# Optimization experiments

Hardware: AMD Instinct MI355X
Metric: run time of the kernel (lower is better)

## Reference

```python
import jax, jax.numpy as jnp
import numpy as np

E = 256        # emb_size / d_model
DI = 512       # d_inner = expand * d_model
N = 16         # d_state
R = 16         # dt_rank = ceil(E/16)
KC = 4         # d_conv


def layer_norm(x, g, b, eps=1e-5):
    m = jnp.mean(x, axis=-1, keepdims=True)
    v = jnp.mean((x - m) ** 2, axis=-1, keepdims=True)
    return (x - m) * jax.lax.rsqrt(v + eps) * g + b


def causal_dw_conv(x, w, b):
    # x: (B,T,DI), w: (DI,KC), b: (DI). torch Conv1d(groups=DI, padding=KC-1)[..., :T]
    T = x.shape[1]
    xp = jnp.pad(x, ((0, 0), (KC - 1, 0), (0, 0)))
    y = sum(xp[:, k:k + T, :] * w[None, None, :, k] for k in range(KC))
    return y + b


def selective_scan(u, dt, A, Bm, Cm, D):
    # u,dt: (B,T,DI); A: (DI,N); Bm,Cm: (B,T,N); D: (DI,)
    dA = jnp.exp(dt[..., None] * A)                       # (B,T,DI,N)
    dBu = dt[..., None] * Bm[:, :, None, :] * u[..., None]

    def step(h, inp):
        dA_t, dBu_t, C_t = inp
        h = dA_t * h + dBu_t                              # (B,DI,N)
        y = jnp.einsum('bdn,bn->bd', h, C_t)
        return h, y

    h0 = jnp.zeros((u.shape[0], DI, N), u.dtype)
    _, ys = jax.lax.scan(step, h0, (jnp.swapaxes(dA, 0, 1), jnp.swapaxes(dBu, 0, 1), jnp.swapaxes(Cm, 0, 1)))
    return jnp.swapaxes(ys, 0, 1) + u * D


def mamba(x, W_in, conv_w, conv_b, W_xproj, W_dt, b_dt, A_log, Dp, W_out):
    xz = x @ W_in.T                                       # (B,T,2*DI)
    xm, z = xz[..., :DI], xz[..., DI:]
    xm = jax.nn.silu(causal_dw_conv(xm, conv_w, conv_b))
    xdbl = xm @ W_xproj.T                                 # (B,T,R+2N)
    dt = jax.nn.softplus(xdbl[..., :R] @ W_dt.T + b_dt)   # (B,T,DI)
    Bm, Cm = xdbl[..., R:R + N], xdbl[..., R + N:]
    A = -jnp.exp(A_log)
    y = selective_scan(xm, dt, A, Bm, Cm, Dp)
    return (y * jax.nn.silu(z)) @ W_out.T


def forward(f_wavlm, f_sinc, ln_w_g, ln_w_b, ln_s_g, ln_s_b, W_wp, b_wp, W_sp, b_sp,
            W_fuse, b_fuse, W_se1, W_se2, ln_f_g, ln_f_b,
            n1_g, n1_b, n2_g, n2_b,
            W_in, conv_w, conv_b, W_xproj, W_dt, b_dt, A_log, Dp, W_out,
            W_ff1, b_ff1, W_ff2, b_ff2):
    # DualStreamFusion
    fw = layer_norm(f_wavlm, ln_w_g, ln_w_b) @ W_wp.T + b_wp   # (B,T1,E)
    fs = layer_norm(f_sinc, ln_s_g, ln_s_b) @ W_sp.T + b_sp    # (B,T2,E)
    B, T1, _ = fw.shape
    # F.interpolate(mode='linear', align_corners=False) == half-pixel linear resize
    fs = jax.image.resize(fs, (B, T1, E), method='linear')
    fc = jnp.concatenate([fw, fs], axis=-1) @ W_fuse.T + b_fuse
    # SE layer
    se = jax.nn.sigmoid(jax.nn.relu(jnp.mean(fc, axis=1) @ W_se1.T) @ W_se2.T)
    fc = fc * se[:, None, :]
    x = layer_norm(fc, ln_f_g, ln_f_b)                          # dropout is eval identity
    # PN_BiMambas_Encoder
    res = x
    xn = layer_norm(x, n1_g, n1_b)
    mp = (W_in, conv_w, conv_b, W_xproj, W_dt, b_dt, A_log, Dp, W_out)
    mf = mamba(xn, *mp)
    mb = jnp.flip(mamba(jnp.flip(xn, axis=1), *mp), axis=1)
    m = layer_norm(mf + mb, n2_g, n2_b)
    ff = jax.nn.gelu(m @ W_ff1.T + b_ff1, approximate=False) @ W_ff2.T + b_ff2
    return ff + res


def setup_inputs() -> dict:
    key = jax.random.key(0)
    ks = jax.random.split(key, 24)
    g = lambda k, s: (jax.random.normal(k, s, jnp.float32) * 0.02)
    d = {
        'f_wavlm': jax.random.normal(ks[0], (4, 1024, 1024), jnp.float32),
        'f_sinc': jax.random.normal(ks[1], (4, 512, 64), jnp.float32),
        'ln_w_g': jnp.ones((1024,)), 'ln_w_b': jnp.zeros((1024,)),
        'ln_s_g': jnp.ones((64,)), 'ln_s_b': jnp.zeros((64,)),
        'W_wp': g(ks[2], (E, 1024)), 'b_wp': jnp.zeros((E,)),
        'W_sp': g(ks[3], (E, 64)), 'b_sp': jnp.zeros((E,)),
        'W_fuse': g(ks[4], (E, 2 * E)), 'b_fuse': jnp.zeros((E,)),
        'W_se1': g(ks[5], (E // 16, E)), 'W_se2': g(ks[6], (E, E // 16)),
        'ln_f_g': jnp.ones((E,)), 'ln_f_b': jnp.zeros((E,)),
        'n1_g': jnp.ones((E,)), 'n1_b': jnp.zeros((E,)),
        'n2_g': jnp.ones((E,)), 'n2_b': jnp.zeros((E,)),
        'W_in': g(ks[7], (2 * DI, E)),
        'conv_w': g(ks[8], (DI, KC)), 'conv_b': jnp.zeros((DI,)),
        'W_xproj': g(ks[9], (R + 2 * N, DI)),
        'W_dt': g(ks[10], (DI, R)), 'b_dt': jnp.full((DI,), -4.6, jnp.float32),
        'A_log': jnp.broadcast_to(jnp.log(jnp.arange(1, N + 1, dtype=jnp.float32)), (DI, N)).copy(),
        'Dp': jnp.ones((DI,)),
        'W_out': g(ks[11], (E, DI)),
        'W_ff1': g(ks[12], (4 * E, E)), 'b_ff1': jnp.zeros((4 * E,)),
        'W_ff2': g(ks[13], (E, 4 * E)), 'b_ff2': jnp.zeros((E,)),
    }
    return d


def reference(f_wavlm, f_sinc, ln_w_g, ln_w_b, ln_s_g, ln_s_b, W_wp, b_wp, W_sp, b_sp,
              W_fuse, b_fuse, W_se1, W_se2, ln_f_g, ln_f_b,
              n1_g, n1_b, n2_g, n2_b,
              W_in, conv_w, conv_b, W_xproj, W_dt, b_dt, A_log, Dp, W_out,
              W_ff1, b_ff1, W_ff2, b_ff2):
    return forward(f_wavlm, f_sinc, ln_w_g, ln_w_b, ln_s_g, ln_s_b, W_wp, b_wp, W_sp, b_sp,
                   W_fuse, b_fuse, W_se1, W_se2, ln_f_g, ln_f_b,
                   n1_g, n1_b, n2_g, n2_b,
                   W_in, conv_w, conv_b, W_xproj, W_dt, b_dt, A_log, Dp, W_out,
                   W_ff1, b_ff1, W_ff2, b_ff2)
```

## Files before the change

### kernel.cpp

```cpp
#include <hip/hip_runtime.h>
#include <math.h>

#define DEV_INLINE __device__ __forceinline__

typedef __attribute__((ext_vector_type(8))) short bf16x8;
typedef __attribute__((ext_vector_type(4))) float f32x4;

struct US4 { unsigned short x, y, z, w; };

DEV_INLINE unsigned short f2bf(float f) {
  union { float f; unsigned u; } v; v.f = f;
  unsigned r = v.u + 0x7fff + ((v.u >> 16) & 1);
  return (unsigned short)(r >> 16);
}
DEV_INLINE float bf2f(unsigned short h) {
  union { unsigned u; float f; } v; v.u = ((unsigned)h) << 16;
  return v.f;
}
DEV_INLINE float softplusf(float x) {
  return x > 20.f ? x : __logf(1.f + __expf(x));
}

static constexpr size_t OFF_XZ   = 0;
static constexpr size_t SUB_LNW  = 0;
static constexpr size_t SUB_LNS  = 2097152;
static constexpr size_t SUB_CAT  = 2162688;
static constexpr size_t SUB_FSB  = 3211264;
static constexpr size_t OFF_UB   = 4194304;
static constexpr size_t OFF_XD   = 6291456;
static constexpr size_t OFF_SP   = 6684672;
static constexpr size_t OFF_SH   = 8781824;
static constexpr size_t OFF_FC   = 10878976;
static constexpr size_t OFF_RES  = 11927552;
static constexpr size_t OFF_XNB  = 12976128;
static constexpr size_t OFF_MB   = 13500416;
static constexpr size_t OFF_FF1B = 14024704;
static constexpr size_t OFF_WB   = 16121856;
static constexpr size_t OFF_SE1  = 16797696;
static constexpr size_t OFF_SE2  = 16814080;

static constexpr size_t WB_WP    = 0;
static constexpr size_t WB_SP    = 262144;
static constexpr size_t WB_FUSE  = 278528;
static constexpr size_t WB_IN    = 409600;
static constexpr size_t WB_XPROJ = 671744;
static constexpr size_t WB_OUT   = 696320;
static constexpr size_t WB_FF1   = 827392;
static constexpr size_t WB_FF2   = 1089536;

__global__ void k_w2bf(const float* __restrict__ w0, const float* __restrict__ w1,
                       const float* __restrict__ w2, const float* __restrict__ w3,
                       const float* __restrict__ w4, const float* __restrict__ w5,
                       const float* __restrict__ w6, const float* __restrict__ w7,
                       unsigned short* __restrict__ dst) {
  int i = blockIdx.x * 256 + threadIdx.x;
  const float* s; size_t dbase; int rel;
  if      (i <  65536) { s = w0; rel = i;          dbase = WB_WP; }
  else if (i <  69632) { s = w1; rel = i -  65536; dbase = WB_SP; }
  else if (i < 102400) { s = w2; rel = i -  69632; dbase = WB_FUSE; }
  else if (i < 167936) { s = w3; rel = i - 102400; dbase = WB_IN; }
  else if (i < 174080) { s = w4; rel = i - 167936; dbase = WB_XPROJ; }
  else if (i < 206848) { s = w5; rel = i - 174080; dbase = WB_OUT; }
  else if (i < 272384) { s = w6; rel = i - 206848; dbase = WB_FF1; }
  else                 { s = w7; rel = i - 272384; dbase = WB_FF2; }
  float4 v = reinterpret_cast<const float4*>(s)[rel];
  US4 o = { f2bf(v.x), f2bf(v.y), f2bf(v.z), f2bf(v.w) };
  reinterpret_cast<US4*>(dst + dbase)[rel] = o;
}

DEV_INLINE float blockSum256(float v) {
  __shared__ float sh[4];
  int lane = threadIdx.x & 63;
  int w    = threadIdx.x >> 6;
#pragma unroll
  for (int o = 32; o; o >>= 1) v += __shfl_down(v, o, 64);
  __syncthreads();
  if (lane == 0) sh[w] = v;
  __syncthreads();
  return sh[0] + sh[1] + sh[2] + sh[3];
}

__global__ void k_layernorm(const float* __restrict__ in, unsigned short* __restrict__ out,
                            const float* __restrict__ g, const float* __restrict__ b,
                            int L) {
  __shared__ float row[1024];
  size_t rid = blockIdx.x;
  const float* x = in + rid * (size_t)L;
  float s = 0.f;
  for (int i = threadIdx.x; i < L; i += 256) { float v = x[i]; row[i] = v; s += v; }
  float mean = blockSum256(s) / (float)L;
  float vs = 0.f;
  for (int i = threadIdx.x; i < L; i += 256) { float d = row[i] - mean; vs += d * d; }
  float var = blockSum256(vs) / (float)L;
  float rstd = rsqrtf(var + 1e-5f);
  for (int i = threadIdx.x; i < L; i += 256)
    out[rid * (size_t)L + i] = f2bf((row[i] - mean) * rstd * g[i] + b[i]);
}

__global__ void k_layernorm2(const float* __restrict__ mo, unsigned short* __restrict__ out,
                             const float* __restrict__ g, const float* __restrict__ b) {
  size_t rid = blockIdx.x;
  int e = threadIdx.x;
  float v = mo[rid * 256 + e] + mo[(rid + 4096) * 256 + e];
  float m1 = blockSum256(v) * (1.f / 256.f);
  float d = v - m1;
  float var = blockSum256(d * d) * (1.f / 256.f);
  out[rid * 256 + e] = f2bf(d * rsqrtf(var + 1e-5f) * g[e] + b[e]);
}

template <int ACT, bool RESADD, bool OUTBF>
__global__ __launch_bounds__(128) void k_mgemm(
    const short* __restrict__ A, int lda,
    const short* __restrict__ W, int ldw,
    const float* __restrict__ bias,
    float* __restrict__ Cf, unsigned short* __restrict__ Cb, int ldc,
    const float* __restrict__ res,
    int M, int N, int K) {
  int l = threadIdx.x & 63, w = threadIdx.x >> 6;
  int bm = blockIdx.y << 6, bn = blockIdx.x << 6;
  int r = l & 15, ko = (l >> 4) << 3;
  const short* Ap = A + (size_t)(bm + (w << 5) + r) * lda + ko;
  const short* Wp = W + (size_t)(bn + r) * ldw + ko;
  f32x4 acc[2][4] = {{{0.f,0.f,0.f,0.f},{0.f,0.f,0.f,0.f},{0.f,0.f,0.f,0.f},{0.f,0.f,0.f,0.f}},
                     {{0.f,0.f,0.f,0.f},{0.f,0.f,0.f,0.f},{0.f,0.f,0.f,0.f},{0.f,0.f,0.f,0.f}}};
#pragma unroll 2
  for (int k0 = 0; k0 < K; k0 += 32) {
    bf16x8 a0 = *reinterpret_cast<const bf16x8*>(Ap + k0);
    bf16x8 a1 = *reinterpret_cast<const bf16x8*>(Ap + (size_t)16 * lda + k0);
#pragma unroll
    for (int t = 0; t < 4; t++) {
      if (bn + t * 16 < N) {
        bf16x8 bv = *reinterpret_cast<const bf16x8*>(Wp + (size_t)(t * 16) * ldw + k0);
        acc[0][t] = __builtin_amdgcn_mfma_f32_16x16x32_bf16(a0, bv, acc[0][t], 0, 0, 0);
        acc[1][t] = __builtin_amdgcn_mfma_f32_16x16x32_bf16(a1, bv, acc[1][t], 0, 0, 0);
      }
    }
  }
#pragma unroll
  for (int mf = 0; mf < 2; mf++) {
#pragma unroll
    for (int t = 0; t < 4; t++) {
      if (bn + t * 16 < N) {
        int n = bn + t * 16 + r;
        float bb = bias ? bias[n] : 0.f;
#pragma unroll
        for (int q = 0; q < 4; q++) {
          int m = bm + (w << 5) + (mf << 4) + ((l >> 4) << 2) + q;
          float v = acc[mf][t][q] + bb;
          if (ACT == 1) v = 0.5f * v * (1.f + erff(v * 0.70710678118f));
          size_t oi = (size_t)m * ldc + n;
          if (OUTBF) {
            Cb[oi] = f2bf(v);
          } else {
            if (RESADD) v += res[oi];
            Cf[oi] = v;
          }
        }
      }
    }
  }
}

__global__ void k_resize(const unsigned short* __restrict__ fs,
                         unsigned short* __restrict__ cat) {
  int idx = blockIdx.x * 256 + threadIdx.x;
  int e = idx & 255, t = (idx >> 8) & 1023, b = idx >> 18;
  int j = t >> 1;
  int j0, j1; float w0, w1;
  if ((t & 1) == 0) { j0 = j > 0 ? j - 1 : 0; j1 = j; w0 = 0.25f; w1 = 0.75f; }
  else              { j0 = j; j1 = j < 511 ? j + 1 : 511; w0 = 0.75f; w1 = 0.25f; }
  float v = w0 * bf2f(fs[((size_t)(b << 9) + j0) * 256 + e]) +
            w1 * bf2f(fs[((size_t)(b << 9) + j1) * 256 + e]);
  cat[((size_t)(b << 10) + t) * 512 + 256 + e] = f2bf(v);
}

__global__ void k_se_part(const float* __restrict__ fc, float* __restrict__ part) {
  int b = blockIdx.y, chunk = blockIdx.x, e = threadIdx.x;
  float s = 0.f;
  for (int j = 0; j < 64; j++) {
    int t = chunk * 64 + j;
    s += fc[((size_t)(b << 10) + t) * 256 + e];
  }
  part[(size_t)(b * 16 + chunk) * 256 + e] = s;
}

__global__ void k_se_fin(const float* __restrict__ part, const float* __restrict__ W1,
                         const float* __restrict__ W2, float* __restrict__ se) {
  int b = blockIdx.x, tid = threadIdx.x;
  __shared__ float mean[256];
  __shared__ float hid[16];
  float s = 0.f;
  for (int c = 0; c < 16; c++) s += part[(size_t)(b * 16 + c) * 256 + tid];
  mean[tid] = s * (1.f / 1024.f);
  __syncthreads();
  int o = tid >> 4, l = tid & 15;
  float p = 0.f;
  for (int e = l; e < 256; e += 16) p += mean[e] * W1[o * 256 + e];
  p += __shfl_xor(p, 1, 64); p += __shfl_xor(p, 2, 64);
  p += __shfl_xor(p, 4, 64); p += __shfl_xor(p, 8, 64);
  if (l == 0) hid[o] = fmaxf(p, 0.f);
  __syncthreads();
  float s2 = 0.f;
  for (int o2 = 0; o2 < 16; o2++) s2 += hid[o2] * W2[tid * 16 + o2];
  se[b * 256 + tid] = 1.f / (1.f + expf(-s2));
}

__global__ void k_se_ln(const float* __restrict__ fc, const float* __restrict__ se,
                        const float* __restrict__ gf, const float* __restrict__ bf,
                        const float* __restrict__ g1, const float* __restrict__ b1,
                        float* __restrict__ xout, unsigned short* __restrict__ xnb) {
  size_t rid = blockIdx.x;
  int b = (int)(rid >> 10);
  int e = threadIdx.x;
  float v = fc[rid * 256 + e] * se[b * 256 + e];
  float m1 = blockSum256(v) * (1.f / 256.f);
  float d = v - m1;
  float var = blockSum256(d * d) * (1.f / 256.f);
  float x = d * rsqrtf(var + 1e-5f) * gf[e] + bf[e];
  xout[rid * 256 + e] = x;
  float m2 = blockSum256(x) * (1.f / 256.f);
  float d2 = x - m2;
  float v2 = blockSum256(d2 * d2) * (1.f / 256.f);
  xnb[rid * 256 + e] = f2bf(d2 * rsqrtf(v2 + 1e-5f) * g1[e] + b1[e]);
}

__global__ void k_conv(const float* __restrict__ xz, const float* __restrict__ cw,
                       const float* __restrict__ cb, unsigned short* __restrict__ ub) {
  int idx = blockIdx.x * 256 + threadIdx.x;
  int d4 = idx & 127, t = (idx >> 7) & 1023, b = idx >> 17;
  int base = d4 << 2;
  f32x4 rr[7];
#pragma unroll
  for (int o = 0; o < 7; o++) {
    int tt = t + o - 3;
    if (tt >= 0 && tt < 1024)
      rr[o] = *reinterpret_cast<const f32x4*>(xz + ((size_t)(b << 10) + tt) * 1024 + base);
    else
      rr[o] = (f32x4){0.f, 0.f, 0.f, 0.f};
  }
  f32x4 wv[4];
#pragma unroll
  for (int dd = 0; dd < 4; dd++)
    wv[dd] = *reinterpret_cast<const f32x4*>(cw + (size_t)(base + dd) * 4);
  f32x4 cbv = *reinterpret_cast<const f32x4*>(cb + base);
  f32x4 acc0 = cbv, acc1 = cbv;
#pragma unroll
  for (int k = 0; k < 4; k++) {
#pragma unroll
    for (int dd = 0; dd < 4; dd++) {
      acc0[dd] += rr[k][dd] * wv[dd][k];
      acc1[dd] += rr[6 - k][dd] * wv[dd][k];
    }
  }
  US4 o0, o1;
  {
    float v0 = acc0[0] / (1.f + expf(-acc0[0]));
    float v1 = acc0[1] / (1.f + expf(-acc0[1]));
    float v2 = acc0[2] / (1.f + expf(-acc0[2]));
    float v3 = acc0[3] / (1.f + expf(-acc0[3]));
    o0 = { f2bf(v0), f2bf(v1), f2bf(v2), f2bf(v3) };
    v0 = acc1[0] / (1.f + expf(-acc1[0]));
    v1 = acc1[1] / (1.f + expf(-acc1[1]));
    v2 = acc1[2] / (1.f + expf(-acc1[2]));
    v3 = acc1[3] / (1.f + expf(-acc1[3]));
    o1 = { f2bf(v0), f2bf(v1), f2bf(v2), f2bf(v3) };
  }
  size_t r0 = ((size_t)(b << 10) + t) * 512 + base;
  size_t r1 = ((size_t)((4 + b) << 10) + t) * 512 + base;
  *reinterpret_cast<US4*>(ub + r0) = o0;
  *reinterpret_cast<US4*>(ub + r1) = o1;
}


__global__ __launch_bounds__(256) void k_scan_a(
    const unsigned short* __restrict__ ub, const float* __restrict__ xdbl,
    const float* __restrict__ A_log, const float* __restrict__ Wdt,
    const float* __restrict__ bdt,
    float* __restrict__ SP, float* __restrict__ SH) {
  int chunk = blockIdx.x, b = blockIdx.y;
  int dir = blockIdx.z >> 1, dhalf = blockIdx.z & 1;
  int d = (dhalf << 8) + threadIdx.x;
  __shared__ float Ds[32][16];
  __shared__ float Bs[32][16];
  for (int i = threadIdx.x; i < 512; i += 256) {
    int j = i >> 4, n = i & 15;
    int s = (chunk << 5) + j;
    int t = dir ? (1023 - s) : s;
    size_t row = ((size_t)((dir * 4 + b) * 1024 + t)) * 48;
    Ds[j][n] = xdbl[row + n];
    Bs[j][n] = xdbl[row + 16 + n];
  }
  float a[16], h[16], P[16], wdt[16];
#pragma unroll
  for (int n = 0; n < 16; n++) {
    a[n] = -__expf(A_log[d * 16 + n]);
    wdt[n] = Wdt[d * 16 + n];
    h[n] = 0.f; P[n] = 1.f;
  }
  float dbias = bdt[d];
  __syncthreads();
  size_t base = (size_t)(dir * 4 + b) * 1024;
  int s0 = chunk << 5;
#define ADDR(j) ((base + (dir ? (1023 - (s0 + (j))) : (s0 + (j)))) * 512 + d)
  float u_n = bf2f(ub[ADDR(0)]);
#pragma unroll 4
  for (int j = 0; j < 32; j++) {
    float uv = u_n;
    if (j < 31) u_n = bf2f(ub[ADDR(j + 1)]);
    float sdt = dbias;
#pragma unroll
    for (int rj = 0; rj < 16; rj++) sdt += Ds[j][rj] * wdt[rj];
    float dtv = softplusf(sdt);
    float c1 = dtv * uv;
    const float4* Bp = reinterpret_cast<const float4*>(&Bs[j][0]);
    float4 b0 = Bp[0], b1 = Bp[1], b2 = Bp[2], b3 = Bp[3];
    float Bv[16] = {b0.x, b0.y, b0.z, b0.w, b1.x, b1.y, b1.z, b1.w,
                    b2.x, b2.y, b2.z, b2.w, b3.x, b3.y, b3.z, b3.w};
#pragma unroll
    for (int n = 0; n < 16; n++) {
      float dA = __expf(dtv * a[n]);
      h[n] = dA * h[n] + c1 * Bv[n];
      P[n] *= dA;
    }
  }
  size_t o = ((size_t)((dir * 4 + b) * 32 + chunk) * 512 + d) * 16;
#pragma unroll
  for (int n = 0; n < 16; n++) { SP[o + n] = P[n]; SH[o + n] = h[n]; }
#undef ADDR
}

__global__ __launch_bounds__(256) void k_scan_mid(float* __restrict__ SP,
                                                  const float* __restrict__ SH) {
  int dir = blockIdx.z, b = blockIdx.y;
  int d = (blockIdx.x << 4) + (threadIdx.x >> 4);
  int n = threadIdx.x & 15;
  const size_t cs = 512 * 16;
  size_t base = ((size_t)(dir * 4 + b) * 32) * cs + (size_t)d * 16 + n;
  float H = 0.f;
  float Pv = SP[base], hE = SH[base];
  for (int c = 0; c < 32; c++) {
    float Pc = Pv, hc = hE;
    if (c < 31) { Pv = SP[base + (c + 1) * cs]; hE = SH[base + (c + 1) * cs]; }
    SP[base + (size_t)c * cs] = H;
    H = Pc * H + hc;
  }
}

__global__ __launch_bounds__(256) void k_scan_b(
    unsigned short* __restrict__ ub, const float* __restrict__ xdbl,
    const float* __restrict__ A_log, const float* __restrict__ Wdt,
    const float* __restrict__ bdt, const float* __restrict__ Dp,
    const float* __restrict__ xz, const float* __restrict__ SP) {
  int chunk = blockIdx.x, b = blockIdx.y;
  int dir = blockIdx.z >> 1, dhalf = blockIdx.z & 1;
  int d = (dhalf << 8) + threadIdx.x;
  __shared__ float Ds[32][16];
  __shared__ float Bs[32][16];
  __shared__ float Cs[32][16];
  for (int i = threadIdx.x; i < 512; i += 256) {
    int j = i >> 4, n = i & 15;
    int s = (chunk << 5) + j;
    int t = dir ? (1023 - s) : s;
    size_t row = ((size_t)((dir * 4 + b) * 1024 + t)) * 48;
    Ds[j][n] = xdbl[row + n];
    Bs[j][n] = xdbl[row + 16 + n];
    Cs[j][n] = xdbl[row + 32 + n];
  }
  float a[16], h[16], wdt[16];
  size_t so = ((size_t)((dir * 4 + b) * 32 + chunk) * 512 + d) * 16;
#pragma unroll
  for (int n = 0; n < 16; n++) {
    a[n] = -__expf(A_log[d * 16 + n]);
    wdt[n] = Wdt[d * 16 + n];
    h[n] = SP[so + n];
  }
  float dbias = bdt[d];
  float Dval = Dp[d];
  __syncthreads();
  size_t base = (size_t)(dir * 4 + b) * 1024;
  size_t zbase = (size_t)b << 10;
  int s0 = chunk << 5;
#define ADDR(j) ((base + (dir ? (1023 - (s0 + (j))) : (s0 + (j)))) * 512 + d)
#define ZADDR(j) ((((zbase + (dir ? (1023 - (s0 + (j))) : (s0 + (j)))) << 10)) + 512 + d)
  float u_n = bf2f(ub[ADDR(0)]);
  float z_n = xz[ZADDR(0)];
#pragma unroll 4
  for (int j = 0; j < 32; j++) {
    float uv = u_n, zv = z_n;
    if (j < 31) { u_n = bf2f(ub[ADDR(j + 1)]); z_n = xz[ZADDR(j + 1)]; }
    float sdt = dbias;
#pragma unroll
    for (int rj = 0; rj < 16; rj++) sdt += Ds[j][rj] * wdt[rj];
    float dtv = softplusf(sdt);
    float c1 = dtv * uv;
    const float4* Bp = reinterpret_cast<const float4*>(&Bs[j][0]);
    const float4* Cp = reinterpret_cast<const float4*>(&Cs[j][0]);
    float4 b0 = Bp[0], b1 = Bp[1], b2 = Bp[2], b3 = Bp[3];
    float4 c0 = Cp[0], c4 = Cp[1], c8 = Cp[2], cc = Cp[3];
    float Bv[16] = {b0.x, b0.y, b0.z, b0.w, b1.x, b1.y, b1.z, b1.w,
                    b2.x, b2.y, b2.z, b2.w, b3.x, b3.y, b3.z, b3.w};
    float Cv[16] = {c0.x, c0.y, c0.z, c0.w, c4.x, c4.y, c4.z, c4.w,
                    c8.x, c8.y, c8.z, c8.w, cc.x, cc.y, cc.z, cc.w};
    float y0 = 0.f, y1 = 0.f, y2 = 0.f, y3 = 0.f;
#pragma unroll
    for (int n = 0; n < 16; n++) {
      float dA = __expf(dtv * a[n]);
      h[n] = dA * h[n] + c1 * Bv[n];
      float p = h[n] * Cv[n];
      if ((n & 3) == 0) y0 += p; else if ((n & 3) == 1) y1 += p;
      else if ((n & 3) == 2) y2 += p; else y3 += p;
    }
    float y = (y0 + y1) + (y2 + y3) + uv * Dval;
    float sig = 1.f / (1.f + expf(-zv));
    ub[ADDR(j)] = f2bf(y * zv * sig);
  }
#undef ADDR
#undef ZADDR
}

static inline void mgemm(hipStream_t st, int act, bool resadd, bool outbf,
                         const void* A, int lda, const void* W, int ldw,
                         const float* bias, void* Cf, void* Cb, int ldc,
                         const float* res, int M, int N, int K) {
  dim3 g((N + 63) / 64, M / 64), bl(128);
  const short* a = (const short*)A;
  const short* w = (const short*)W;
  float* cf = (float*)Cf;
  unsigned short* cb = (unsigned short*)Cb;
  if (outbf) {
    if (act == 1) hipLaunchKernelGGL((k_mgemm<1, false, true>), g, bl, 0, st, a, lda, w, ldw, bias, cf, cb, ldc, res, M, N, K);
    else          hipLaunchKernelGGL((k_mgemm<0, false, true>), g, bl, 0, st, a, lda, w, ldw, bias, cf, cb, ldc, res, M, N, K);
  } else {
    if (resadd)   hipLaunchKernelGGL((k_mgemm<0, true, false>), g, bl, 0, st, a, lda, w, ldw, bias, cf, cb, ldc, res, M, N, K);
    else          hipLaunchKernelGGL((k_mgemm<0, false, false>), g, bl, 0, st, a, lda, w, ldw, bias, cf, cb, ldc, res, M, N, K);
  }
}

extern "C" void kernel_launch(void* const* d_in, const int* in_sizes, int n_in,
                              void* d_out, int out_size, void* d_ws, size_t ws_size,
                              hipStream_t stream) {
  const float* f_wavlm = (const float*)d_in[0];
  const float* f_sinc  = (const float*)d_in[1];
  const float* ln_w_g  = (const float*)d_in[2];
  const float* ln_w_b  = (const float*)d_in[3];
  const float* ln_s_g  = (const float*)d_in[4];
  const float* ln_s_b  = (const float*)d_in[5];
  const float* W_wp    = (const float*)d_in[6];
  const float* b_wp    = (const float*)d_in[7];
  const float* W_sp    = (const float*)d_in[8];
  const float* b_sp    = (const float*)d_in[9];
  const float* W_fuse  = (const float*)d_in[10];
  const float* b_fuse  = (const float*)d_in[11];
  const float* W_se1   = (const float*)d_in[12];
  const float* W_se2   = (const float*)d_in[13];
  const float* ln_f_g  = (const float*)d_in[14];
  const float* ln_f_b  = (const float*)d_in[15];
  const float* n1_g    = (const float*)d_in[16];
  const float* n1_b    = (const float*)d_in[17];
  const float* n2_g    = (const float*)d_in[18];
  const float* n2_b    = (const float*)d_in[19];
  const float* W_in    = (const float*)d_in[20];
  const float* conv_w  = (const float*)d_in[21];
  const float* conv_b  = (const float*)d_in[22];
  const float* W_xproj = (const float*)d_in[23];
  const float* W_dt    = (const float*)d_in[24];
  const float* b_dt    = (const float*)d_in[25];
  const float* A_log   = (const float*)d_in[26];
  const float* Dp      = (const float*)d_in[27];
  const float* W_out   = (const float*)d_in[28];
  const float* W_ff1   = (const float*)d_in[29];
  const float* b_ff1   = (const float*)d_in[30];
  const float* W_ff2   = (const float*)d_in[31];
  const float* b_ff2   = (const float*)d_in[32];

  float* ws = (float*)d_ws;
  float* pXZ  = ws + OFF_XZ;
  unsigned short* pLNW = (unsigned short*)(ws + SUB_LNW);
  unsigned short* pLNS = (unsigned short*)(ws + SUB_LNS);
  unsigned short* pCAT = (unsigned short*)(ws + SUB_CAT);
  unsigned short* pFSB = (unsigned short*)(ws + SUB_FSB);
  unsigned short* pUB  = (unsigned short*)(ws + OFF_UB);
  float* pXD  = ws + OFF_XD;
  float* pSP  = ws + OFF_SP;
  float* pMO  = ws + OFF_SP;
  float* pSH  = ws + OFF_SH;
  float* pFC  = ws + OFF_FC;
  float* pRES = ws + OFF_RES;
  unsigned short* pXNB  = (unsigned short*)(ws + OFF_XNB);
  unsigned short* pMB   = (unsigned short*)(ws + OFF_MB);
  unsigned short* pFF1B = (unsigned short*)(ws + OFF_FF1B);
  unsigned short* pWB   = (unsigned short*)(ws + OFF_WB);
  float* pSE1 = ws + OFF_SE1;
  float* pSE2 = ws + OFF_SE2;

  hipLaunchKernelGGL(k_w2bf, dim3(1320), dim3(256), 0, stream,
                     W_wp, W_sp, W_fuse, W_in, W_xproj, W_out, W_ff1, W_ff2, pWB);

  hipLaunchKernelGGL(k_layernorm, dim3(4096), dim3(256), 0, stream,
                     f_wavlm, pLNW, ln_w_g, ln_w_b, 1024);
  mgemm(stream, 0, false, true, pLNW, 1024, pWB + WB_WP, 1024, b_wp,
        nullptr, pCAT, 512, nullptr, 4096, 256, 1024);

  hipLaunchKernelGGL(k_layernorm, dim3(2048), dim3(256), 0, stream,
                     f_sinc, pLNS, ln_s_g, ln_s_b, 64);
  mgemm(stream, 0, false, true, pLNS, 64, pWB + WB_SP, 64, b_sp,
        nullptr, pFSB, 256, nullptr, 2048, 256, 64);

  hipLaunchKernelGGL(k_resize, dim3(4096), dim3(256), 0, stream, pFSB, pCAT);
  mgemm(stream, 0, false, false, pCAT, 512, pWB + WB_FUSE, 512, b_fuse,
        pFC, nullptr, 256, nullptr, 4096, 256, 512);

  hipLaunchKernelGGL(k_se_part, dim3(16, 4), dim3(256), 0, stream, pFC, pSE1);
  hipLaunchKernelGGL(k_se_fin, dim3(4), dim3(256), 0, stream, pSE1, W_se1, W_se2, pSE2);

  hipLaunchKernelGGL(k_se_ln, dim3(4096), dim3(256), 0, stream,
                     pFC, pSE2, ln_f_g, ln_f_b, n1_g, n1_b, pRES, pXNB);

  mgemm(stream, 0, false, false, pXNB, 256, pWB + WB_IN, 256, nullptr,
        pXZ, nullptr, 1024, nullptr, 4096, 1024, 256);

  hipLaunchKernelGGL(k_conv, dim3(2048), dim3(256), 0, stream,
                     pXZ, conv_w, conv_b, pUB);

  mgemm(stream, 0, false, false, pUB, 512, pWB + WB_XPROJ, 512, nullptr,
        pXD, nullptr, 48, nullptr, 8192, 48, 512);

  hipLaunchKernelGGL(k_scan_a, dim3(32, 4, 4), dim3(256), 0, stream,
                     pUB, pXD, A_log, W_dt, b_dt, pSP, pSH);
  hipLaunchKernelGGL(k_scan_mid, dim3(32, 4, 2), dim3(256), 0, stream, pSP, pSH);
  hipLaunchKernelGGL(k_scan_b, dim3(32, 4, 4), dim3(256), 0, stream,
                     pUB, pXD, A_log, W_dt, b_dt, Dp, pXZ, pSP);

  mgemm(stream, 0, false, false, pUB, 512, pWB + WB_OUT, 512, nullptr,
        pMO, nullptr, 256, nullptr, 8192, 256, 512);
  hipLaunchKernelGGL(k_layernorm2, dim3(4096), dim3(256), 0, stream, pMO, pMB, n2_g, n2_b);

  mgemm(stream, 1, false, true, pMB, 256, pWB + WB_FF1, 256, b_ff1,
        nullptr, pFF1B, 1024, nullptr, 4096, 1024, 256);
  mgemm(stream, 0, true, false, pFF1B, 1024, pWB + WB_FF2, 1024, b_ff2,
        d_out, nullptr, 256, pRES, 4096, 256, 1024);
}
```

Measured before the change: 402.0 us.

## Split GEMM K across waves with LDS reduction; fuse z-silu into in-proj epilogue

The MFMA GEMM now uses 256-thread blocks. It splits the K dimension across 4 waves (or 2 waves for small K) and reduces the partial accumulators through shared memory, which adds waves per output tile and improves latency hiding. The in-projection GEMM gains a split output mode: the xm half goes to fp32 and silu(z) goes to a bf16 buffer, so the scan's final kernel reads half the bytes and skips the sigmoid. The costs are extra LDS traffic and a __syncthreads per tile. The K=64 GEMM with KS=2 and the N=48 case depend on the guard logic.

```diff
diff --git a/kernel.cpp b/kernel.cpp
--- a/kernel.cpp
+++ b/kernel.cpp
@@ -26,6 +26,8 @@
 static constexpr size_t SUB_LNS  = 2097152;
 static constexpr size_t SUB_CAT  = 2162688;
 static constexpr size_t SUB_FSB  = 3211264;
+static constexpr size_t SUB_XM   = 0;
+static constexpr size_t SUB_ZB   = 2097152;
 static constexpr size_t OFF_UB   = 4194304;
 static constexpr size_t OFF_XD   = 6291456;
 static constexpr size_t OFF_SP   = 6684672;
@@ -108,23 +110,28 @@
   out[rid * 256 + e] = f2bf(d * rsqrtf(var + 1e-5f) * g[e] + b[e]);
 }
 
-template <int ACT, bool RESADD, bool OUTBF>
-__global__ __launch_bounds__(128) void k_mgemm(
+template <int ACT, bool RESADD, int OUTMODE, int KS>
+__global__ __launch_bounds__(256) void k_mgemm(
     const short* __restrict__ A, int lda,
     const short* __restrict__ W, int ldw,
     const float* __restrict__ bias,
     float* __restrict__ Cf, unsigned short* __restrict__ Cb, int ldc,
     const float* __restrict__ res,
     int M, int N, int K) {
+  __shared__ float red[(KS == 2 ? 2 : 3)][32][65];
   int l = threadIdx.x & 63, w = threadIdx.x >> 6;
-  int bm = blockIdx.y << 6, bn = blockIdx.x << 6;
-  int r = l & 15, ko = (l >> 4) << 3;
-  const short* Ap = A + (size_t)(bm + (w << 5) + r) * lda + ko;
-  const short* Wp = W + (size_t)(bn + r) * ldw + ko;
+  int wm = (KS == 2) ? (w & 1) : 0;
+  int wk = (KS == 2) ? (w >> 1) : w;
+  int bm = (KS == 2) ? ((blockIdx.y << 6) + (wm << 5)) : (blockIdx.y << 5);
+  int bn = blockIdx.x << 6;
+  int r = l & 15, rrow = (l >> 4) << 2, ko = (l >> 4) << 3;
+  int KH = K / KS;
+  const short* Ap = A + (size_t)(bm + r) * lda + wk * KH + ko;
+  const short* Wp = W + (size_t)(bn + r) * ldw + wk * KH + ko;
   f32x4 acc[2][4] = {{{0.f,0.f,0.f,0.f},{0.f,0.f,0.f,0.f},{0.f,0.f,0.f,0.f},{0.f,0.f,0.f,0.f}},
                      {{0.f,0.f,0.f,0.f},{0.f,0.f,0.f,0.f},{0.f,0.f,0.f,0.f},{0.f,0.f,0.f,0.f}}};
 #pragma unroll 2
-  for (int k0 = 0; k0 < K; k0 += 32) {
+  for (int k0 = 0; k0 < KH; k0 += 32) {
     bf16x8 a0 = *reinterpret_cast<const bf16x8*>(Ap + k0);
     bf16x8 a1 = *reinterpret_cast<const bf16x8*>(Ap + (size_t)16 * lda + k0);
 #pragma unroll
@@ -136,24 +143,44 @@
       }
     }
   }
-#pragma unroll
-  for (int mf = 0; mf < 2; mf++) {
-#pragma unroll
-    for (int t = 0; t < 4; t++) {
-      if (bn + t * 16 < N) {
-        int n = bn + t * 16 + r;
-        float bb = bias ? bias[n] : 0.f;
-#pragma unroll
-        for (int q = 0; q < 4; q++) {
-          int m = bm + (w << 5) + (mf << 4) + ((l >> 4) << 2) + q;
-          float v = acc[mf][t][q] + bb;
-          if (ACT == 1) v = 0.5f * v * (1.f + erff(v * 0.70710678118f));
-          size_t oi = (size_t)m * ldc + n;
-          if (OUTBF) {
-            Cb[oi] = f2bf(v);
-          } else {
-            if (RESADD) v += res[oi];
-            Cf[oi] = v;
+  if (wk > 0) {
+    int slot = (KS == 2) ? wm : (wk - 1);
+#pragma unroll
+    for (int mf = 0; mf < 2; mf++)
+#pragma unroll
+      for (int t = 0; t < 4; t++)
+#pragma unroll
+        for (int q = 0; q < 4; q++)
+          red[slot][(mf << 4) + rrow + q][t * 16 + r] = acc[mf][t][q];
+  }
+  __syncthreads();
+  if (wk == 0) {
+#pragma unroll
+    for (int mf = 0; mf < 2; mf++) {
+#pragma unroll
+      for (int t = 0; t < 4; t++) {
+        if (bn + t * 16 < N) {
+          int n = bn + t * 16 + r;
+          float bb = bias ? bias[n] : 0.f;
+#pragma unroll
+          for (int q = 0; q < 4; q++) {
+            int rw = (mf << 4) + rrow + q, cl = t * 16 + r;
+            float v = acc[mf][t][q];
+            if (KS == 2) v += red[wm][rw][cl];
+            else         v += red[0][rw][cl] + red[1][rw][cl] + red[2][rw][cl];
+            v += bb;
+            if (ACT == 1) v = 0.5f * v * (1.f + erff(v * 0.70710678118f));
+            int m = bm + rw;
+            if (OUTMODE == 0) {
+              size_t oi = (size_t)m * ldc + n;
+              if (RESADD) v += res[oi];
+              Cf[oi] = v;
+            } else if (OUTMODE == 1) {
+              Cb[(size_t)m * ldc + n] = f2bf(v);
+            } else {
+              if (n < 512) Cf[(size_t)m * 512 + n] = v;
+              else Cb[(size_t)m * 512 + (n - 512)] = f2bf(v / (1.f + __expf(-v)));
+            }
           }
         }
       }
@@ -224,7 +251,7 @@
   xnb[rid * 256 + e] = f2bf(d2 * rsqrtf(v2 + 1e-5f) * g1[e] + b1[e]);
 }
 
-__global__ void k_conv(const float* __restrict__ xz, const float* __restrict__ cw,
+__global__ void k_conv(const float* __restrict__ xm, const float* __restrict__ cw,
                        const float* __restrict__ cb, unsigned short* __restrict__ ub) {
   int idx = blockIdx.x * 256 + threadIdx.x;
   int d4 = idx & 127, t = (idx >> 7) & 1023, b = idx >> 17;
@@ -234,7 +261,7 @@
   for (int o = 0; o < 7; o++) {
     int tt = t + o - 3;
     if (tt >= 0 && tt < 1024)
-      rr[o] = *reinterpret_cast<const f32x4*>(xz + ((size_t)(b << 10) + tt) * 1024 + base);
+      rr[o] = *reinterpret_cast<const f32x4*>(xm + ((size_t)(b << 10) + tt) * 512 + base);
     else
       rr[o] = (f32x4){0.f, 0.f, 0.f, 0.f};
   }
@@ -270,7 +297,6 @@
   *reinterpret_cast<US4*>(ub + r0) = o0;
   *reinterpret_cast<US4*>(ub + r1) = o1;
 }
-
 
 __global__ __launch_bounds__(256) void k_scan_a(
     const unsigned short* __restrict__ ub, const float* __restrict__ xdbl,
@@ -350,7 +376,7 @@
     unsigned short* __restrict__ ub, const float* __restrict__ xdbl,
     const float* __restrict__ A_log, const float* __restrict__ Wdt,
     const float* __restrict__ bdt, const float* __restrict__ Dp,
-    const float* __restrict__ xz, const float* __restrict__ SP) {
+    const unsigned short* __restrict__ zb, const float* __restrict__ SP) {
   int chunk = blockIdx.x, b = blockIdx.y;
   int dir = blockIdx.z >> 1, dhalf = blockIdx.z & 1;
   int d = (dhalf << 8) + threadIdx.x;
@@ -381,13 +407,13 @@
   size_t zbase = (size_t)b << 10;
   int s0 = chunk << 5;
 #define ADDR(j) ((base + (dir ? (1023 - (s0 + (j))) : (s0 + (j)))) * 512 + d)
-#define ZADDR(j) ((((zbase + (dir ? (1023 - (s0 + (j))) : (s0 + (j)))) << 10)) + 512 + d)
+#define ZADDR(j) (((zbase + (dir ? (1023 - (s0 + (j))) : (s0 + (j)))) * 512) + d)
   float u_n = bf2f(ub[ADDR(0)]);
-  float z_n = xz[ZADDR(0)];
+  float z_n = bf2f(zb[ZADDR(0)]);
 #pragma unroll 4
   for (int j = 0; j < 32; j++) {
-    float uv = u_n, zv = z_n;
-    if (j < 31) { u_n = bf2f(ub[ADDR(j + 1)]); z_n = xz[ZADDR(j + 1)]; }
+    float uv = u_n, szv = z_n;
+    if (j < 31) { u_n = bf2f(ub[ADDR(j + 1)]); z_n = bf2f(zb[ZADDR(j + 1)]); }
     float sdt = dbias;
 #pragma unroll
     for (int rj = 0; rj < 16; rj++) sdt += Ds[j][rj] * wdt[rj];
@@ -411,28 +437,31 @@
       else if ((n & 3) == 2) y2 += p; else y3 += p;
     }
     float y = (y0 + y1) + (y2 + y3) + uv * Dval;
-    float sig = 1.f / (1.f + expf(-zv));
-    ub[ADDR(j)] = f2bf(y * zv * sig);
+    ub[ADDR(j)] = f2bf(y * szv);
   }
 #undef ADDR
 #undef ZADDR
 }
 
-static inline void mgemm(hipStream_t st, int act, bool resadd, bool outbf,
+static inline void mgemm(hipStream_t st, int act, bool resadd, int outmode,
                          const void* A, int lda, const void* W, int ldw,
                          const float* bias, void* Cf, void* Cb, int ldc,
                          const float* res, int M, int N, int K) {
-  dim3 g((N + 63) / 64, M / 64), bl(128);
+  bool ks4 = (K >= 256);
+  dim3 g((N + 63) / 64, ks4 ? (M / 32) : (M / 64)), bl(256);
   const short* a = (const short*)A;
   const short* w = (const short*)W;
   float* cf = (float*)Cf;
   unsigned short* cb = (unsigned short*)Cb;
-  if (outbf) {
-    if (act == 1) hipLaunchKernelGGL((k_mgemm<1, false, true>), g, bl, 0, st, a, lda, w, ldw, bias, cf, cb, ldc, res, M, N, K);
-    else          hipLaunchKernelGGL((k_mgemm<0, false, true>), g, bl, 0, st, a, lda, w, ldw, bias, cf, cb, ldc, res, M, N, K);
+  if (outmode == 2) {
+    hipLaunchKernelGGL((k_mgemm<0, false, 2, 4>), g, bl, 0, st, a, lda, w, ldw, bias, cf, cb, ldc, res, M, N, K);
+  } else if (outmode == 1) {
+    if (act == 1)      hipLaunchKernelGGL((k_mgemm<1, false, 1, 4>), g, bl, 0, st, a, lda, w, ldw, bias, cf, cb, ldc, res, M, N, K);
+    else if (ks4)      hipLaunchKernelGGL((k_mgemm<0, false, 1, 4>), g, bl, 0, st, a, lda, w, ldw, bias, cf, cb, ldc, res, M, N, K);
+    else               hipLaunchKernelGGL((k_mgemm<0, false, 1, 2>), g, bl, 0, st, a, lda, w, ldw, bias, cf, cb, ldc, res, M, N, K);
   } else {
-    if (resadd)   hipLaunchKernelGGL((k_mgemm<0, true, false>), g, bl, 0, st, a, lda, w, ldw, bias, cf, cb, ldc, res, M, N, K);
-    else          hipLaunchKernelGGL((k_mgemm<0, false, false>), g, bl, 0, st, a, lda, w, ldw, bias, cf, cb, ldc, res, M, N, K);
+    if (resadd)        hipLaunchKernelGGL((k_mgemm<0, true, 0, 4>), g, bl, 0, st, a, lda, w, ldw, bias, cf, cb, ldc, res, M, N, K);
+    else               hipLaunchKernelGGL((k_mgemm<0, false, 0, 4>), g, bl, 0, st, a, lda, w, ldw, bias, cf, cb, ldc, res, M, N, K);
   }
 }
 
@@ -474,11 +503,12 @@
   const float* b_ff2   = (const float*)d_in[32];
 
   float* ws = (float*)d_ws;
-  float* pXZ  = ws + OFF_XZ;
   unsigned short* pLNW = (unsigned short*)(ws + SUB_LNW);
   unsigned short* pLNS = (unsigned short*)(ws + SUB_LNS);
   unsigned short* pCAT = (unsigned short*)(ws + SUB_CAT);
   unsigned short* pFSB = (unsigned short*)(ws + SUB_FSB);
+  float* pXM = ws + SUB_XM;
+  unsigned short* pZB = (unsigned short*)(ws + SUB_ZB);
   unsigned short* pUB  = (unsigned short*)(ws + OFF_UB);
   float* pXD  = ws + OFF_XD;
   float* pSP  = ws + OFF_SP;
@@ -498,16 +528,16 @@
 
   hipLaunchKernelGGL(k_layernorm, dim3(4096), dim3(256), 0, stream,
                      f_wavlm, pLNW, ln_w_g, ln_w_b, 1024);
-  mgemm(stream, 0, false, true, pLNW, 1024, pWB + WB_WP, 1024, b_wp,
+  mgemm(stream, 0, false, 1, pLNW, 1024, pWB + WB_WP, 1024, b_wp,
         nullptr, pCAT, 512, nullptr, 4096, 256, 1024);
 
   hipLaunchKernelGGL(k_layernorm, dim3(2048), dim3(256), 0, stream,
                      f_sinc, pLNS, ln_s_g, ln_s_b, 64);
-  mgemm(stream, 0, false, true, pLNS, 64, pWB + WB_SP, 64, b_sp,
+  mgemm(stream, 0, false, 1, pLNS, 64, pWB + WB_SP, 64, b_sp,
         nullptr, pFSB, 256, nullptr, 2048, 256, 64);
 
   hipLaunchKernelGGL(k_resize, dim3(4096), dim3(256), 0, stream, pFSB, pCAT);
-  mgemm(stream, 0, false, false, pCAT, 512, pWB + WB_FUSE, 512, b_fuse,
+  mgemm(stream, 0, false, 0, pCAT, 512, pWB + WB_FUSE, 512, b_fuse,
         pFC, nullptr, 256, nullptr, 4096, 256, 512);
 
   hipLaunchKernelGGL(k_se_part, dim3(16, 4), dim3(256), 0, stream, pFC, pSE1);
@@ -516,27 +546,27 @@
   hipLaunchKernelGGL(k_se_ln, dim3(4096), dim3(256), 0, stream,
                      pFC, pSE2, ln_f_g, ln_f_b, n1_g, n1_b, pRES, pXNB);
 
-  mgemm(stream, 0, false, false, pXNB, 256, pWB + WB_IN, 256, nullptr,
-        pXZ, nullptr, 1024, nullptr, 4096, 1024, 256);
+  mgemm(stream, 0, false, 2, pXNB, 256, pWB + WB_IN, 256, nullptr,
+        pXM, pZB, 512, nullptr, 4096, 1024, 256);
 
   hipLaunchKernelGGL(k_conv, dim3(2048), dim3(256), 0, stream,
-                     pXZ, conv_w, conv_b, pUB);
-
-  mgemm(stream, 0, false, false, pUB, 512, pWB + WB_XPROJ, 512, nullptr,
+                     pXM, conv_w, conv_b, pUB);
+
+  mgemm(stream, 0, false, 0, pUB, 512, pWB + WB_XPROJ, 512, nullptr,
         pXD, nullptr, 48, nullptr, 8192, 48, 512);
 
   hipLaunchKernelGGL(k_scan_a, dim3(32, 4, 4), dim3(256), 0, stream,
                      pUB, pXD, A_log, W_dt, b_dt, pSP, pSH);
   hipLaunchKernelGGL(k_scan_mid, dim3(32, 4, 2), dim3(256), 0, stream, pSP, pSH);
   hipLaunchKernelGGL(k_scan_b, dim3(32, 4, 4), dim3(256), 0, stream,
-                     pUB, pXD, A_log, W_dt, b_dt, Dp, pXZ, pSP);
-
-  mgemm(stream, 0, false, false, pUB, 512, pWB + WB_OUT, 512, nullptr,
+                     pUB, pXD, A_log, W_dt, b_dt, Dp, pZB, pSP);
+
+  mgemm(stream, 0, false, 0, pUB, 512, pWB + WB_OUT, 512, nullptr,
         pMO, nullptr, 256, nullptr, 8192, 256, 512);
   hipLaunchKernelGGL(k_layernorm2, dim3(4096), dim3(256), 0, stream, pMO, pMB, n2_g, n2_b);
 
-  mgemm(stream, 1, false, true, pMB, 256, pWB + WB_FF1, 256, b_ff1,
+  mgemm(stream, 1, false, 1, pMB, 256, pWB + WB_FF1, 256, b_ff1,
         nullptr, pFF1B, 1024, nullptr, 4096, 1024, 256);
-  mgemm(stream, 0, true, false, pFF1B, 1024, pWB + WB_FF2, 1024, b_ff2,
+  mgemm(stream, 0, true, 0, pFF1B, 1024, pWB + WB_FF2, 1024, b_ff2,
         d_out, nullptr, 256, pRES, 4096, 256, 1024);
 }
```

Result: faster. 359.9 us (-10.5%).
